# Performance work log

Measured on AMD Instinct MI355X. Metric: run time of the kernel, lower is better.

## Reference

```python
import jax, jax.numpy as jnp
import numpy as np

B, S, D, H = 2, 2048, 1024, 16
HD = D // H  # head_dim = 64


def setup_inputs() -> dict:
    key = jax.random.key(0)
    ks = jax.random.split(key, 5)
    scale = 1.0 / np.sqrt(D)
    return {
        "x": jax.random.normal(ks[0], (B, S, D), jnp.float32),
        "Wq": jax.random.normal(ks[1], (D, D), jnp.float32) * scale,
        "Wk": jax.random.normal(ks[2], (D, D), jnp.float32) * scale,
        "Wv": jax.random.normal(ks[3], (D, D), jnp.float32) * scale,
        "Wo": jax.random.normal(ks[4], (D, D), jnp.float32) * scale,
        "bo": jnp.zeros((D,), jnp.float32),
    }


def reference(x, Wq, Wk, Wv, Wo, bo):
    b, s, d = x.shape
    # torch nn.Linear: y = x @ W.T  (W stored [d_out, d_in])
    q = (x @ Wq.T).reshape(b, s, H, HD).transpose(0, 2, 1, 3)  # [b,h,s,hd]
    k = (x @ Wk.T).reshape(b, s, H, HD).transpose(0, 2, 1, 3)
    v = (x @ Wv.T).reshape(b, s, H, HD).transpose(0, 2, 1, 3)
    scores = jnp.einsum("bhqd,bhkd->bhqk", q, k) / jnp.sqrt(jnp.float32(HD))
    causal = jnp.triu(jnp.ones((s, s), dtype=bool), k=1)
    scores = jnp.where(causal[None, None], -jnp.inf, scores)
    attn = jax.nn.softmax(scores, axis=-1)
    ctx = jnp.einsum("bhqk,bhkd->bhqd", attn, v)
    ctx = ctx.transpose(0, 2, 1, 3).reshape(b, s, d)
    return ctx @ Wo.T + bo
```

## Files before the change

kernel.cpp:

```cpp
#include <hip/hip_runtime.h>

#define B_  2
#define S_  2048
#define D_  1024
#define H_  16
#define HD_ 64
#define M_  4096

typedef __attribute__((ext_vector_type(8))) short  short8;
typedef __attribute__((ext_vector_type(4))) float  floatx4;

__device__ __forceinline__ unsigned short f2bf(float f) {
  unsigned int u = __float_as_uint(f);
  u = (u + 0x7fffu + ((u >> 16) & 1u)) >> 16;
  return (unsigned short)u;
}

__device__ __forceinline__ void gl_lds16(const short* g, short* l) {
  __builtin_amdgcn_global_load_lds(
      (const __attribute__((address_space(1))) unsigned int*)g,
      (__attribute__((address_space(3))) unsigned int*)l, 16, 0, 0);
}

__global__ __launch_bounds__(256) void cast_kernel(
    const float* __restrict__ x,  const float* __restrict__ wq,
    const float* __restrict__ wk, const float* __restrict__ wv,
    const float* __restrict__ wo,
    short* __restrict__ xb,  short* __restrict__ wqb, short* __restrict__ wkb,
    short* __restrict__ wvb, short* __restrict__ wob) {
  const float* src; short* dst; int n8;
  switch (blockIdx.y) {
    case 0:  src = x;  dst = xb;  n8 = (M_ * D_) / 8; break;
    case 1:  src = wq; dst = wqb; n8 = (D_ * D_) / 8; break;
    case 2:  src = wk; dst = wkb; n8 = (D_ * D_) / 8; break;
    case 3:  src = wv; dst = wvb; n8 = (D_ * D_) / 8; break;
    default: src = wo; dst = wob; n8 = (D_ * D_) / 8; break;
  }
  int i = blockIdx.x * 256 + threadIdx.x;
  if (i >= n8) return;
  float4 a = ((const float4*)src)[2 * i];
  float4 b = ((const float4*)src)[2 * i + 1];
  short8 o;
  o[0] = (short)f2bf(a.x); o[1] = (short)f2bf(a.y);
  o[2] = (short)f2bf(a.z); o[3] = (short)f2bf(a.w);
  o[4] = (short)f2bf(b.x); o[5] = (short)f2bf(b.y);
  o[6] = (short)f2bf(b.z); o[7] = (short)f2bf(b.w);
  ((short8*)dst)[i] = o;
}

__global__ __launch_bounds__(256) void gemm_qkv(
    const short* __restrict__ xb,  const short* __restrict__ wqb,
    const short* __restrict__ wkb, const short* __restrict__ wvb,
    short* __restrict__ qo, short* __restrict__ ko, short* __restrict__ vto) {
  __shared__ alignas(16) short As[128 * 32];
  __shared__ alignas(16) short Bs[128 * 32];
  const int tid  = threadIdx.x;
  const int lane = tid & 63, wid = tid >> 6;
  const int quad = lane >> 4, l16 = lane & 15;
  const int bn = blockIdx.x, bm = blockIdx.y, z = blockIdx.z;
  const short* wsel = (z == 0) ? wqb : ((z == 1) ? wkb : wvb);
  const float scale = (z == 0) ? 0.125f * 1.44269504f : 1.0f;
  const int lrow = wid * 32 + (lane >> 2);
  const int lcol = (lane & 3) * 8;
  const short* ag0 = xb   + (bm * 128 + lrow) * D_ + lcol;
  const short* ag1 = ag0 + 16 * D_;
  const short* bg0 = wsel + (bn * 128 + lrow) * D_ + lcol;
  const short* bg1 = bg0 + 16 * D_;
  short* la0 = &As[(wid * 32) * 32];
  short* la1 = &As[(wid * 32 + 16) * 32];
  short* lb0 = &Bs[(wid * 32) * 32];
  short* lb1 = &Bs[(wid * 32 + 16) * 32];
  const int wm = (wid & 1) * 64, wn = (wid >> 1) * 64;
  floatx4 acc[4][4];
#pragma unroll
  for (int i = 0; i < 4; i++)
#pragma unroll
    for (int j = 0; j < 4; j++) acc[i][j] = (floatx4){0.f, 0.f, 0.f, 0.f};

  for (int k0 = 0; k0 < D_; k0 += 32) {
    __syncthreads();
    gl_lds16(ag0 + k0, la0);
    gl_lds16(ag1 + k0, la1);
    gl_lds16(bg0 + k0, lb0);
    gl_lds16(bg1 + k0, lb1);
    __syncthreads();
    short8 af[4], bf[4];
#pragma unroll
    for (int t = 0; t < 4; t++) af[t] = *(const short8*)&As[(wm + t * 16 + l16) * 32 + quad * 8];
#pragma unroll
    for (int t = 0; t < 4; t++) bf[t] = *(const short8*)&Bs[(wn + t * 16 + l16) * 32 + quad * 8];
#pragma unroll
    for (int tm = 0; tm < 4; tm++)
#pragma unroll
      for (int tn = 0; tn < 4; tn++)
        acc[tm][tn] = __builtin_amdgcn_mfma_f32_16x16x32_bf16(af[tm], bf[tn], acc[tm][tn], 0, 0, 0);
  }
#pragma unroll
  for (int tm = 0; tm < 4; tm++) {
#pragma unroll
    for (int tn = 0; tn < 4; tn++) {
      int n = bn * 128 + wn + tn * 16 + l16;
      int h = n >> 6, hd = n & 63;
#pragma unroll
      for (int r = 0; r < 4; r++) {
        int m = bm * 128 + wm + tm * 16 + quad * 4 + r;
        int b = m >> 11, s = m & 2047;
        unsigned short val = f2bf(acc[tm][tn][r] * scale);
        if (z == 2)
          vto[((b * H_ + h) * HD_ + hd) * S_ + s] = (short)val;
        else if (z == 1)
          ko[((b * H_ + h) * S_ + s) * HD_ + hd] = (short)val;
        else
          qo[((b * H_ + h) * S_ + s) * HD_ + hd] = (short)val;
      }
    }
  }
}

__global__ __launch_bounds__(256) void gemm_out(
    const short* __restrict__ cx, const short* __restrict__ wob,
    const float* __restrict__ bo, float* __restrict__ out) {
  __shared__ alignas(16) short As[128 * 32];
  __shared__ alignas(16) short Bs[128 * 32];
  const int tid  = threadIdx.x;
  const int lane = tid & 63, wid = tid >> 6;
  const int quad = lane >> 4, l16 = lane & 15;
  const int bn = blockIdx.x, bm = blockIdx.y;
  const int lrow = wid * 32 + (lane >> 2);
  const int lcol = (lane & 3) * 8;
  const short* ag0 = cx  + (bm * 128 + lrow) * D_ + lcol;
  const short* ag1 = ag0 + 16 * D_;
  const short* bg0 = wob + (bn * 128 + lrow) * D_ + lcol;
  const short* bg1 = bg0 + 16 * D_;
  short* la0 = &As[(wid * 32) * 32];
  short* la1 = &As[(wid * 32 + 16) * 32];
  short* lb0 = &Bs[(wid * 32) * 32];
  short* lb1 = &Bs[(wid * 32 + 16) * 32];
  const int wm = (wid & 1) * 64, wn = (wid >> 1) * 64;
  floatx4 acc[4][4];
#pragma unroll
  for (int i = 0; i < 4; i++)
#pragma unroll
    for (int j = 0; j < 4; j++) acc[i][j] = (floatx4){0.f, 0.f, 0.f, 0.f};

  for (int k0 = 0; k0 < D_; k0 += 32) {
    __syncthreads();
    gl_lds16(ag0 + k0, la0);
    gl_lds16(ag1 + k0, la1);
    gl_lds16(bg0 + k0, lb0);
    gl_lds16(bg1 + k0, lb1);
    __syncthreads();
    short8 af[4], bf[4];
#pragma unroll
    for (int t = 0; t < 4; t++) af[t] = *(const short8*)&As[(wm + t * 16 + l16) * 32 + quad * 8];
#pragma unroll
    for (int t = 0; t < 4; t++) bf[t] = *(const short8*)&Bs[(wn + t * 16 + l16) * 32 + quad * 8];
#pragma unroll
    for (int tm = 0; tm < 4; tm++)
#pragma unroll
      for (int tn = 0; tn < 4; tn++)
        acc[tm][tn] = __builtin_amdgcn_mfma_f32_16x16x32_bf16(af[tm], bf[tn], acc[tm][tn], 0, 0, 0);
  }
#pragma unroll
  for (int tn = 0; tn < 4; tn++) {
    int n = bn * 128 + wn + tn * 16 + l16;
    float bias = bo[n];
#pragma unroll
    for (int tm = 0; tm < 4; tm++) {
#pragma unroll
      for (int r = 0; r < 4; r++) {
        int m = bm * 128 + wm + tm * 16 + quad * 4 + r;
        out[m * D_ + n] = acc[tm][tn][r] + bias;
      }
    }
  }
}

__global__ __launch_bounds__(256) void attn_kernel(
    const short* __restrict__ qbuf, const short* __restrict__ kbuf,
    const short* __restrict__ vtbuf, short* __restrict__ ctx) {
  __shared__ alignas(16) short Ks[64][72];
  __shared__ alignas(16) short Vs[64][72];
  __shared__ alignas(16) short Ps[4][16][72];
  const int tid  = threadIdx.x;
  const int lane = tid & 63, wid = tid >> 6;
  const int quad = lane >> 4, l16 = lane & 15;
  const int bx = blockIdx.x, by = blockIdx.y;
  const int qblk = ((by >> 3) & 1) ? bx : (31 - bx);
  const int bh = by;
  const int base = bh * (S_ * HD_);
  const int q0 = qblk * 64 + wid * 16;

  short8 qf0 = *(const short8*)(qbuf + base + (q0 + l16) * HD_ + quad * 8);
  short8 qf1 = *(const short8*)(qbuf + base + (q0 + l16) * HD_ + 32 + quad * 8);

  float lsum[4];
  floatx4 o[4];
#pragma unroll
  for (int r = 0; r < 4; r++) lsum[r] = 0.f;
#pragma unroll
  for (int nt = 0; nt < 4; nt++) o[nt] = (floatx4){0.f, 0.f, 0.f, 0.f};

  const int row = tid >> 2, c8 = (tid & 3) * 16;
  const short* kg = kbuf  + base + row * HD_ + c8;
  const short* vg = vtbuf + base + row * S_  + c8;
  short8 kv0 = *(const short8*)(kg);
  short8 kv1 = *(const short8*)(kg + 8);
  short8 vv0 = *(const short8*)(vg);
  short8 vv1 = *(const short8*)(vg + 8);

  for (int kt = 0; kt <= qblk; kt++) {
    __syncthreads();
    *(short8*)&Ks[row][c8]     = kv0;
    *(short8*)&Ks[row][c8 + 8] = kv1;
    *(short8*)&Vs[row][c8]     = vv0;
    *(short8*)&Vs[row][c8 + 8] = vv1;
    __syncthreads();
    {
      const int ktn = (kt < qblk) ? kt + 1 : kt;
      const short* kgn = kg + ktn * 64 * HD_;
      const short* vgn = vg + ktn * 64;
      kv0 = *(const short8*)(kgn);
      kv1 = *(const short8*)(kgn + 8);
      vv0 = *(const short8*)(vgn);
      vv1 = *(const short8*)(vgn + 8);
    }

    floatx4 sc[4];
#pragma unroll
    for (int ct = 0; ct < 4; ct++) {
      short8 kb0 = *(const short8*)&Ks[ct * 16 + l16][quad * 8];
      short8 kb1 = *(const short8*)&Ks[ct * 16 + l16][32 + quad * 8];
      floatx4 zz = (floatx4){0.f, 0.f, 0.f, 0.f};
      zz     = __builtin_amdgcn_mfma_f32_16x16x32_bf16(qf0, kb0, zz, 0, 0, 0);
      sc[ct] = __builtin_amdgcn_mfma_f32_16x16x32_bf16(qf1, kb1, zz, 0, 0, 0);
    }
    if (kt == qblk) {
#pragma unroll
      for (int ct = 0; ct < 4; ct++)
#pragma unroll
        for (int r = 0; r < 4; r++)
          if (ct * 16 + l16 > wid * 16 + quad * 4 + r) sc[ct][r] = -INFINITY;
    }
#pragma unroll
    for (int r = 0; r < 4; r++) {
#pragma unroll
      for (int ct = 0; ct < 4; ct++) {
        float p = __builtin_amdgcn_exp2f(sc[ct][r] - 32.0f);
        lsum[r] += p;
        Ps[wid][quad * 4 + r][ct * 16 + l16] = (short)(__float_as_uint(p) >> 16);
      }
    }
#pragma unroll
    for (int ks = 0; ks < 2; ks++) {
      short8 pa = *(const short8*)&Ps[wid][l16][ks * 32 + quad * 8];
#pragma unroll
      for (int nt = 0; nt < 4; nt++) {
        short8 vb = *(const short8*)&Vs[nt * 16 + l16][ks * 32 + quad * 8];
        o[nt] = __builtin_amdgcn_mfma_f32_16x16x32_bf16(pa, vb, o[nt], 0, 0, 0);
      }
    }
  }
#pragma unroll
  for (int r = 0; r < 4; r++) {
    float ls = lsum[r];
    ls += __shfl_xor(ls, 1);
    ls += __shfl_xor(ls, 2);
    ls += __shfl_xor(ls, 4);
    ls += __shfl_xor(ls, 8);
    float linv = 1.f / ls;
    int s = q0 + quad * 4 + r;
    int rowbase = ((bh >> 4) * S_ + s) * D_ + (bh & 15) * HD_;
#pragma unroll
    for (int nt = 0; nt < 4; nt++)
      ctx[rowbase + nt * 16 + l16] = (short)f2bf(o[nt][r] * linv);
  }
}

extern "C" void kernel_launch(void* const* d_in, const int* in_sizes, int n_in,
                              void* d_out, int out_size, void* d_ws, size_t ws_size,
                              hipStream_t stream) {
  const float* x  = (const float*)d_in[0];
  const float* wq = (const float*)d_in[1];
  const float* wk = (const float*)d_in[2];
  const float* wv = (const float*)d_in[3];
  const float* wo = (const float*)d_in[4];
  const float* bo = (const float*)d_in[5];
  float* out = (float*)d_out;

  char* ws = (char*)d_ws;
  short* xb  = (short*)(ws);
  short* wqb = (short*)(ws + (8u  << 20));
  short* wkb = (short*)(ws + (10u << 20));
  short* wvb = (short*)(ws + (12u << 20));
  short* wob = (short*)(ws + (14u << 20));
  short* qb  = (short*)(ws + (16u << 20));
  short* kb  = (short*)(ws + (24u << 20));
  short* cx  = (short*)(ws + (32u << 20));
  short* vtb = (short*)(ws + (40u << 20));

  cast_kernel<<<dim3(2048, 5), 256, 0, stream>>>(x, wq, wk, wv, wo, xb, wqb, wkb, wvb, wob);
  gemm_qkv   <<<dim3(8, 32, 3), 256, 0, stream>>>(xb, wqb, wkb, wvb, qb, kb, vtb);
  attn_kernel<<<dim3(32, 32),   256, 0, stream>>>(qb, kb, vtb, cx);
  gemm_out   <<<dim3(8, 32),    256, 0, stream>>>(cx, wob, bo, out);
}
```

Before: 189.0 us.

## Shrink GEMM N-tile to 64 and double attention query tile per block

Both GEMMs now use 128x64 block tiles (each warp 64x32), which doubles the grid and aims to fill more of the MI355X's compute units, at the cost of less B-tile reuse. The attention kernel now processes 128 queries per block (32 per warp), so each K/V tile staged in LDS serves twice as many queries and the number of blocks is halved. Per-warp causal skipping and masking are added for the larger tile. The risks are lower occupancy in the attention kernel, higher register pressure, and warps idling at the diagonal tiles.

Measured after the change: 209.8 us. +11.0%, slower.

```diff
diff --git a/kernel.cpp b/kernel.cpp
--- a/kernel.cpp
+++ b/kernel.cpp
@@ -53,53 +53,51 @@
     const short* __restrict__ wkb, const short* __restrict__ wvb,
     short* __restrict__ qo, short* __restrict__ ko, short* __restrict__ vto) {
   __shared__ alignas(16) short As[128 * 32];
-  __shared__ alignas(16) short Bs[128 * 32];
+  __shared__ alignas(16) short Bs[64 * 32];
   const int tid  = threadIdx.x;
   const int lane = tid & 63, wid = tid >> 6;
   const int quad = lane >> 4, l16 = lane & 15;
   const int bn = blockIdx.x, bm = blockIdx.y, z = blockIdx.z;
   const short* wsel = (z == 0) ? wqb : ((z == 1) ? wkb : wvb);
   const float scale = (z == 0) ? 0.125f * 1.44269504f : 1.0f;
-  const int lrow = wid * 32 + (lane >> 2);
-  const int lcol = (lane & 3) * 8;
-  const short* ag0 = xb   + (bm * 128 + lrow) * D_ + lcol;
+  const int arow = wid * 32 + (lane >> 2);
+  const int acol = (lane & 3) * 8;
+  const short* ag0 = xb + (bm * 128 + arow) * D_ + acol;
   const short* ag1 = ag0 + 16 * D_;
-  const short* bg0 = wsel + (bn * 128 + lrow) * D_ + lcol;
-  const short* bg1 = bg0 + 16 * D_;
+  const int brow = wid * 16 + (lane >> 2);
+  const short* bg0 = wsel + (bn * 64 + brow) * D_ + acol;
   short* la0 = &As[(wid * 32) * 32];
   short* la1 = &As[(wid * 32 + 16) * 32];
-  short* lb0 = &Bs[(wid * 32) * 32];
-  short* lb1 = &Bs[(wid * 32 + 16) * 32];
-  const int wm = (wid & 1) * 64, wn = (wid >> 1) * 64;
-  floatx4 acc[4][4];
+  short* lb0 = &Bs[(wid * 16) * 32];
+  const int wm = (wid & 1) * 64, wn = (wid >> 1) * 32;
+  floatx4 acc[4][2];
 #pragma unroll
   for (int i = 0; i < 4; i++)
 #pragma unroll
-    for (int j = 0; j < 4; j++) acc[i][j] = (floatx4){0.f, 0.f, 0.f, 0.f};
+    for (int j = 0; j < 2; j++) acc[i][j] = (floatx4){0.f, 0.f, 0.f, 0.f};
 
   for (int k0 = 0; k0 < D_; k0 += 32) {
     __syncthreads();
     gl_lds16(ag0 + k0, la0);
     gl_lds16(ag1 + k0, la1);
     gl_lds16(bg0 + k0, lb0);
-    gl_lds16(bg1 + k0, lb1);
-    __syncthreads();
-    short8 af[4], bf[4];
+    __syncthreads();
+    short8 af[4], bf[2];
 #pragma unroll
     for (int t = 0; t < 4; t++) af[t] = *(const short8*)&As[(wm + t * 16 + l16) * 32 + quad * 8];
 #pragma unroll
-    for (int t = 0; t < 4; t++) bf[t] = *(const short8*)&Bs[(wn + t * 16 + l16) * 32 + quad * 8];
+    for (int t = 0; t < 2; t++) bf[t] = *(const short8*)&Bs[(wn + t * 16 + l16) * 32 + quad * 8];
 #pragma unroll
     for (int tm = 0; tm < 4; tm++)
 #pragma unroll
-      for (int tn = 0; tn < 4; tn++)
+      for (int tn = 0; tn < 2; tn++)
         acc[tm][tn] = __builtin_amdgcn_mfma_f32_16x16x32_bf16(af[tm], bf[tn], acc[tm][tn], 0, 0, 0);
   }
 #pragma unroll
   for (int tm = 0; tm < 4; tm++) {
 #pragma unroll
-    for (int tn = 0; tn < 4; tn++) {
-      int n = bn * 128 + wn + tn * 16 + l16;
+    for (int tn = 0; tn < 2; tn++) {
+      int n = bn * 64 + wn + tn * 16 + l16;
       int h = n >> 6, hd = n & 63;
 #pragma unroll
       for (int r = 0; r < 4; r++) {
@@ -121,49 +119,47 @@
     const short* __restrict__ cx, const short* __restrict__ wob,
     const float* __restrict__ bo, float* __restrict__ out) {
   __shared__ alignas(16) short As[128 * 32];
-  __shared__ alignas(16) short Bs[128 * 32];
+  __shared__ alignas(16) short Bs[64 * 32];
   const int tid  = threadIdx.x;
   const int lane = tid & 63, wid = tid >> 6;
   const int quad = lane >> 4, l16 = lane & 15;
   const int bn = blockIdx.x, bm = blockIdx.y;
-  const int lrow = wid * 32 + (lane >> 2);
-  const int lcol = (lane & 3) * 8;
-  const short* ag0 = cx  + (bm * 128 + lrow) * D_ + lcol;
+  const int arow = wid * 32 + (lane >> 2);
+  const int acol = (lane & 3) * 8;
+  const short* ag0 = cx + (bm * 128 + arow) * D_ + acol;
   const short* ag1 = ag0 + 16 * D_;
-  const short* bg0 = wob + (bn * 128 + lrow) * D_ + lcol;
-  const short* bg1 = bg0 + 16 * D_;
+  const int brow = wid * 16 + (lane >> 2);
+  const short* bg0 = wob + (bn * 64 + brow) * D_ + acol;
   short* la0 = &As[(wid * 32) * 32];
   short* la1 = &As[(wid * 32 + 16) * 32];
-  short* lb0 = &Bs[(wid * 32) * 32];
-  short* lb1 = &Bs[(wid * 32 + 16) * 32];
-  const int wm = (wid & 1) * 64, wn = (wid >> 1) * 64;
-  floatx4 acc[4][4];
+  short* lb0 = &Bs[(wid * 16) * 32];
+  const int wm = (wid & 1) * 64, wn = (wid >> 1) * 32;
+  floatx4 acc[4][2];
 #pragma unroll
   for (int i = 0; i < 4; i++)
 #pragma unroll
-    for (int j = 0; j < 4; j++) acc[i][j] = (floatx4){0.f, 0.f, 0.f, 0.f};
+    for (int j = 0; j < 2; j++) acc[i][j] = (floatx4){0.f, 0.f, 0.f, 0.f};
 
   for (int k0 = 0; k0 < D_; k0 += 32) {
     __syncthreads();
     gl_lds16(ag0 + k0, la0);
     gl_lds16(ag1 + k0, la1);
     gl_lds16(bg0 + k0, lb0);
-    gl_lds16(bg1 + k0, lb1);
-    __syncthreads();
-    short8 af[4], bf[4];
+    __syncthreads();
+    short8 af[4], bf[2];
 #pragma unroll
     for (int t = 0; t < 4; t++) af[t] = *(const short8*)&As[(wm + t * 16 + l16) * 32 + quad * 8];
 #pragma unroll
-    for (int t = 0; t < 4; t++) bf[t] = *(const short8*)&Bs[(wn + t * 16 + l16) * 32 + quad * 8];
+    for (int t = 0; t < 2; t++) bf[t] = *(const short8*)&Bs[(wn + t * 16 + l16) * 32 + quad * 8];
 #pragma unroll
     for (int tm = 0; tm < 4; tm++)
 #pragma unroll
-      for (int tn = 0; tn < 4; tn++)
+      for (int tn = 0; tn < 2; tn++)
         acc[tm][tn] = __builtin_amdgcn_mfma_f32_16x16x32_bf16(af[tm], bf[tn], acc[tm][tn], 0, 0, 0);
   }
 #pragma unroll
-  for (int tn = 0; tn < 4; tn++) {
-    int n = bn * 128 + wn + tn * 16 + l16;
+  for (int tn = 0; tn < 2; tn++) {
+    int n = bn * 64 + wn + tn * 16 + l16;
     float bias = bo[n];
 #pragma unroll
     for (int tm = 0; tm < 4; tm++) {
@@ -181,25 +177,29 @@
     const short* __restrict__ vtbuf, short* __restrict__ ctx) {
   __shared__ alignas(16) short Ks[64][72];
   __shared__ alignas(16) short Vs[64][72];
-  __shared__ alignas(16) short Ps[4][16][72];
+  __shared__ alignas(16) short Ps[4][32][72];
   const int tid  = threadIdx.x;
   const int lane = tid & 63, wid = tid >> 6;
   const int quad = lane >> 4, l16 = lane & 15;
   const int bx = blockIdx.x, by = blockIdx.y;
-  const int qblk = ((by >> 3) & 1) ? bx : (31 - bx);
+  const int qtile = ((by >> 4) & 1) ? bx : (15 - bx);
   const int bh = by;
   const int base = bh * (S_ * HD_);
-  const int q0 = qblk * 64 + wid * 16;
-
-  short8 qf0 = *(const short8*)(qbuf + base + (q0 + l16) * HD_ + quad * 8);
-  short8 qf1 = *(const short8*)(qbuf + base + (q0 + l16) * HD_ + 32 + quad * 8);
-
-  float lsum[4];
-  floatx4 o[4];
-#pragma unroll
-  for (int r = 0; r < 4; r++) lsum[r] = 0.f;
-#pragma unroll
-  for (int nt = 0; nt < 4; nt++) o[nt] = (floatx4){0.f, 0.f, 0.f, 0.f};
+  const int q0 = qtile * 128 + wid * 32;
+
+  short8 qf[2][2];
+#pragma unroll
+  for (int ms = 0; ms < 2; ms++) {
+    qf[ms][0] = *(const short8*)(qbuf + base + (q0 + ms * 16 + l16) * HD_ + quad * 8);
+    qf[ms][1] = *(const short8*)(qbuf + base + (q0 + ms * 16 + l16) * HD_ + 32 + quad * 8);
+  }
+
+  float lsum[2][4];
+  floatx4 o[2][4];
+#pragma unroll
+  for (int ms = 0; ms < 2; ms++)
+#pragma unroll
+    for (int r = 0; r < 4; r++) { lsum[ms][r] = 0.f; o[ms][r] = (floatx4){0.f, 0.f, 0.f, 0.f}; }
 
   const int row = tid >> 2, c8 = (tid & 3) * 16;
   const short* kg = kbuf  + base + row * HD_ + c8;
@@ -209,7 +209,8 @@
   short8 vv0 = *(const short8*)(vg);
   short8 vv1 = *(const short8*)(vg + 8);
 
-  for (int kt = 0; kt <= qblk; kt++) {
+  const int nkt = 2 * (qtile + 1);
+  for (int kt = 0; kt < nkt; kt++) {
     __syncthreads();
     *(short8*)&Ks[row][c8]     = kv0;
     *(short8*)&Ks[row][c8 + 8] = kv1;
@@ -217,7 +218,7 @@
     *(short8*)&Vs[row][c8 + 8] = vv1;
     __syncthreads();
     {
-      const int ktn = (kt < qblk) ? kt + 1 : kt;
+      const int ktn = (kt + 1 < nkt) ? kt + 1 : kt;
       const short* kgn = kg + ktn * 64 * HD_;
       const short* vgn = vg + ktn * 64;
       kv0 = *(const short8*)(kgn);
@@ -225,56 +226,72 @@
       vv0 = *(const short8*)(vgn);
       vv1 = *(const short8*)(vgn + 8);
     }
-
-    floatx4 sc[4];
-#pragma unroll
-    for (int ct = 0; ct < 4; ct++) {
-      short8 kb0 = *(const short8*)&Ks[ct * 16 + l16][quad * 8];
-      short8 kb1 = *(const short8*)&Ks[ct * 16 + l16][32 + quad * 8];
-      floatx4 zz = (floatx4){0.f, 0.f, 0.f, 0.f};
-      zz     = __builtin_amdgcn_mfma_f32_16x16x32_bf16(qf0, kb0, zz, 0, 0, 0);
-      sc[ct] = __builtin_amdgcn_mfma_f32_16x16x32_bf16(qf1, kb1, zz, 0, 0, 0);
-    }
-    if (kt == qblk) {
-#pragma unroll
-      for (int ct = 0; ct < 4; ct++)
+    if (kt * 64 <= q0 + 31) {
+      floatx4 sc[2][4];
+#pragma unroll
+      for (int ct = 0; ct < 4; ct++) {
+        short8 kb0 = *(const short8*)&Ks[ct * 16 + l16][quad * 8];
+        short8 kb1 = *(const short8*)&Ks[ct * 16 + l16][32 + quad * 8];
+#pragma unroll
+        for (int ms = 0; ms < 2; ms++) {
+          floatx4 zz = (floatx4){0.f, 0.f, 0.f, 0.f};
+          zz          = __builtin_amdgcn_mfma_f32_16x16x32_bf16(qf[ms][0], kb0, zz, 0, 0, 0);
+          sc[ms][ct]  = __builtin_amdgcn_mfma_f32_16x16x32_bf16(qf[ms][1], kb1, zz, 0, 0, 0);
+        }
+      }
+#pragma unroll
+      for (int ms = 0; ms < 2; ms++) {
+        if (kt * 64 + 63 > q0 + ms * 16) {
+#pragma unroll
+          for (int ct = 0; ct < 4; ct++)
+#pragma unroll
+            for (int r = 0; r < 4; r++)
+              if (kt * 64 + ct * 16 + l16 > q0 + ms * 16 + quad * 4 + r)
+                sc[ms][ct][r] = -INFINITY;
+        }
+      }
+#pragma unroll
+      for (int ms = 0; ms < 2; ms++)
 #pragma unroll
         for (int r = 0; r < 4; r++)
-          if (ct * 16 + l16 > wid * 16 + quad * 4 + r) sc[ct][r] = -INFINITY;
-    }
+#pragma unroll
+          for (int ct = 0; ct < 4; ct++) {
+            float p = __builtin_amdgcn_exp2f(sc[ms][ct][r] - 32.0f);
+            lsum[ms][r] += p;
+            Ps[wid][ms * 16 + quad * 4 + r][ct * 16 + l16] = (short)(__float_as_uint(p) >> 16);
+          }
+#pragma unroll
+      for (int ks = 0; ks < 2; ks++) {
+        short8 vb[4];
+#pragma unroll
+        for (int nt = 0; nt < 4; nt++)
+          vb[nt] = *(const short8*)&Vs[nt * 16 + l16][ks * 32 + quad * 8];
+#pragma unroll
+        for (int ms = 0; ms < 2; ms++) {
+          short8 pa = *(const short8*)&Ps[wid][ms * 16 + l16][ks * 32 + quad * 8];
+#pragma unroll
+          for (int nt = 0; nt < 4; nt++)
+            o[ms][nt] = __builtin_amdgcn_mfma_f32_16x16x32_bf16(pa, vb[nt], o[ms][nt], 0, 0, 0);
+        }
+      }
+    }
+  }
+#pragma unroll
+  for (int ms = 0; ms < 2; ms++)
 #pragma unroll
     for (int r = 0; r < 4; r++) {
-#pragma unroll
-      for (int ct = 0; ct < 4; ct++) {
-        float p = __builtin_amdgcn_exp2f(sc[ct][r] - 32.0f);
-        lsum[r] += p;
-        Ps[wid][quad * 4 + r][ct * 16 + l16] = (short)(__float_as_uint(p) >> 16);
-      }
-    }
-#pragma unroll
-    for (int ks = 0; ks < 2; ks++) {
-      short8 pa = *(const short8*)&Ps[wid][l16][ks * 32 + quad * 8];
-#pragma unroll
-      for (int nt = 0; nt < 4; nt++) {
-        short8 vb = *(const short8*)&Vs[nt * 16 + l16][ks * 32 + quad * 8];
-        o[nt] = __builtin_amdgcn_mfma_f32_16x16x32_bf16(pa, vb, o[nt], 0, 0, 0);
-      }
-    }
-  }
-#pragma unroll
-  for (int r = 0; r < 4; r++) {
-    float ls = lsum[r];
-    ls += __shfl_xor(ls, 1);
-    ls += __shfl_xor(ls, 2);
-    ls += __shfl_xor(ls, 4);
-    ls += __shfl_xor(ls, 8);
-    float linv = 1.f / ls;
-    int s = q0 + quad * 4 + r;
-    int rowbase = ((bh >> 4) * S_ + s) * D_ + (bh & 15) * HD_;
-#pragma unroll
-    for (int nt = 0; nt < 4; nt++)
-      ctx[rowbase + nt * 16 + l16] = (short)f2bf(o[nt][r] * linv);
-  }
+      float ls = lsum[ms][r];
+      ls += __shfl_xor(ls, 1);
+      ls += __shfl_xor(ls, 2);
+      ls += __shfl_xor(ls, 4);
+      ls += __shfl_xor(ls, 8);
+      float linv = 1.f / ls;
+      int s = q0 + ms * 16 + quad * 4 + r;
+      int rowbase = ((bh >> 4) * S_ + s) * D_ + (bh & 15) * HD_;
+#pragma unroll
+      for (int nt = 0; nt < 4; nt++)
+        ctx[rowbase + nt * 16 + l16] = (short)f2bf(o[ms][nt][r] * linv);
+    }
 }
 
 extern "C" void kernel_launch(void* const* d_in, const int* in_sizes, int n_in,
@@ -299,8 +316,8 @@
   short* cx  = (short*)(ws + (32u << 20));
   short* vtb = (short*)(ws + (40u << 20));
 
-  cast_kernel<<<dim3(2048, 5), 256, 0, stream>>>(x, wq, wk, wv, wo, xb, wqb, wkb, wvb, wob);
-  gemm_qkv   <<<dim3(8, 32, 3), 256, 0, stream>>>(xb, wqb, wkb, wvb, qb, kb, vtb);
-  attn_kernel<<<dim3(32, 32),   256, 0, stream>>>(qb, kb, vtb, cx);
-  gemm_out   <<<dim3(8, 32),    256, 0, stream>>>(cx, wob, bo, out);
-}
+  cast_kernel<<<dim3(2048, 5),  256, 0, stream>>>(x, wq, wk, wv, wo, xb, wqb, wkb, wvb, wob);
+  gemm_qkv   <<<dim3(16, 32, 3), 256, 0, stream>>>(xb, wqb, wkb, wvb, qb, kb, vtb);
+  attn_kernel<<<dim3(16, 32),   256, 0, stream>>>(qb, kb, vtb, cx);
+  gemm_out   <<<dim3(16, 32),   256, 0, stream>>>(cx, wob, bo, out);
+}
```
